# Optimization experiments

Measured on AMD Instinct MI355X. Metric: run time of the kernel, lower is better.

## Reference

```python
import jax, jax.numpy as jnp
import numpy as np

N_NODES = 20000
N_EDGES = 320000
F_DIM = 64      # num_features == hidden_units
HID = 64
N_RUNS = 10
N_GRAPHS = 128
N_CLASSES = 10
N_LAYERS = 4
BN_EPS = 1e-5
P_DROP = 0.2


def _batchnorm(t, g, b):
    # training-mode BatchNorm1d over the flattened (num_runs*N, d) rows, biased variance
    mu = jnp.mean(t, axis=0)
    var = jnp.mean(jnp.square(t - mu), axis=0)
    return (t - mu) * jax.lax.rsqrt(var + BN_EPS) * g + b


def setup_inputs() -> dict:
    key = jax.random.key(0)
    ks = jax.random.split(key, 16)
    x = jax.random.normal(ks[0], (N_NODES, F_DIM), jnp.float32)
    edge_index = jax.random.randint(ks[1], (2, N_EDGES), 0, N_NODES, dtype=jnp.int32)
    batch = jnp.sort(jax.random.randint(ks[2], (N_NODES,), 0, N_GRAPHS, dtype=jnp.int32))
    drop_mask = jax.random.uniform(ks[3], (N_RUNS, N_NODES)) < P_DROP
    s = 0.1
    conv_w1 = jax.random.normal(ks[4], (N_LAYERS, F_DIM, HID), jnp.float32) * s
    conv_b1 = jax.random.normal(ks[5], (N_LAYERS, HID), jnp.float32) * s
    bn1_g = jax.random.uniform(ks[6], (N_LAYERS, HID), jnp.float32, 0.5, 1.5)
    bn1_b = jax.random.normal(ks[7], (N_LAYERS, HID), jnp.float32) * s
    conv_w2 = jax.random.normal(ks[8], (N_LAYERS, HID, HID), jnp.float32) * s
    conv_b2 = jax.random.normal(ks[9], (N_LAYERS, HID), jnp.float32) * s
    bn_g = jax.random.uniform(ks[10], (N_LAYERS, HID), jnp.float32, 0.5, 1.5)
    bn_b = jax.random.normal(ks[11], (N_LAYERS, HID), jnp.float32) * s
    fc_w = jax.random.normal(ks[12], (N_LAYERS + 1, HID, N_CLASSES), jnp.float32) * s
    fc_b = jax.random.normal(ks[13], (N_LAYERS + 1, N_CLASSES), jnp.float32) * s
    return dict(x=x, edge_index=edge_index, batch=batch, drop_mask=drop_mask,
                conv_w1=conv_w1, conv_b1=conv_b1, bn1_g=bn1_g, bn1_b=bn1_b,
                conv_w2=conv_w2, conv_b2=conv_b2, bn_g=bn_g, bn_b=bn_b,
                fc_w=fc_w, fc_b=fc_b)


def reference(x, edge_index, batch, drop_mask,
              conv_w1, conv_b1, bn1_g, bn1_b, conv_w2, conv_b2, bn_g, bn_b,
              fc_w, fc_b):
    # prediction path (eval): node-drop, 4 GIN layers over num_runs replicated
    # graphs, per-level mean-over-runs + global_add_pool + fc, sum, log_softmax.
    R = drop_mask.shape[0]
    N = x.shape[0]
    src, dst = edge_index[0], edge_index[1]
    # replicated node features with stochastic node drop: [R, N, F]
    h = jnp.where(drop_mask[..., None], jnp.zeros((), x.dtype), x[None])
    outs = [h]
    for i in range(N_LAYERS):
        # GINConv (eps=0): MLP(x + sum_{j->i} x_j); vectorized over runs
        # (equivalent to the original offset-replicated run_edge_index).
        agg = jnp.zeros_like(h).at[:, dst].add(h[:, src])  # [R, N, d]
        z = (h + agg).reshape(R * N, -1)
        t = z @ conv_w1[i] + conv_b1[i]
        t = jax.nn.relu(_batchnorm(t, bn1_g[i], bn1_b[i]))
        t = t @ conv_w2[i] + conv_b2[i]
        t = jax.nn.relu(_batchnorm(t, bn_g[i], bn_b[i]))
        h = t.reshape(R, N, -1)
        outs.append(h)
    out = jnp.zeros((N_GRAPHS, N_CLASSES), x.dtype)
    for i, o in enumerate(outs):
        m = jnp.mean(o, axis=0)  # [N, d] mean over runs
        pooled = jax.ops.segment_sum(m, batch, num_segments=N_GRAPHS)  # global_add_pool
        out = out + pooled @ fc_w[i] + fc_b[i]  # dropout is identity in eval
    return jax.nn.log_softmax(out, axis=-1)
```

## Files before the change

kernel.cpp:

```cpp
#include <hip/hip_runtime.h>

#define N_NODES 20000
#define N_EDGES 320000
#define R_RUNS 10
#define HID 64
#define NG 128
#define NC 10
#define NL 4
#define MROWS (R_RUNS * N_NODES)
#define BN_EPS 1e-5f
#define NCOPY 16

typedef __bf16 bf16;
typedef __attribute__((ext_vector_type(8))) __bf16 bf16x8;
typedef __attribute__((ext_vector_type(4))) float f32x4;
typedef unsigned int uint32;

constexpr size_t OFF_FLAGS   = 0;
constexpr size_t OFF_CURSOR  = 256;
constexpr size_t OFF_STATS   = 80384;
constexpr size_t OFF_POOLED5 = 145920;
constexpr size_t ZERO_BYTES  = 309760;
constexpr size_t OFF_ROWST   = 309760;
constexpr size_t OFF_COL     = 389888;
constexpr size_t OFF_PARAMS  = 1669888;
constexpr size_t OFF_XB      = 1745152;
constexpr size_t OFF_H       = 4305152;
constexpr size_t OFF_Z       = 29905152;

#define PW1  0
#define PB1  16384
#define PG1  16640
#define PBB1 16896
#define PW2  17152
#define PB2  33536
#define PG2  33792
#define PBB2 34048
#define PFW  34304
#define PFB  37504
#define PTOT 37554
#define CVT_TOT (1280000 + PTOT)

__global__ void detect_kernel(const unsigned short* __restrict__ xu,
                              const unsigned int* __restrict__ mw,
                              int* __restrict__ cnts) {
    int tid = blockIdx.x * 256 + threadIdx.x;
    int insane = 0, lowp = 0, f32w = 0, gt1 = 0;
    for (int i = tid; i < 4096; i += 16384) {
        unsigned int u = xu[2 * i];
        if (((u >> 7) & 0xFFu) >= 0x90u) insane++;
    }
    for (int i = tid; i < 50000; i += 16384) {
        unsigned int w = mw[i];
        if ((w & 0xFFFFu) == 0x3F80u) lowp = 1;
        else if (w == 0x3F800000u) f32w = 1;
        else if (w > 1u) gt1 = 1;
    }
    if (insane) atomicAdd(&cnts[0], insane);
    if (lowp)   atomicOr(&cnts[1], 1);
    if (f32w)   atomicOr(&cnts[2], 1);
    if (gt1)    atomicOr(&cnts[3], 1);
}

__device__ inline bf16 ld_any(const void* p, int i, int f32mode) {
    if (f32mode) return (bf16)((const float*)p)[i];
    return ((const bf16*)p)[i];
}

__global__ void convert_kernel(const int* __restrict__ cnts,
                               const void* x, const void* w1, const void* b1,
                               const void* g1, const void* bb1, const void* w2,
                               const void* b2, const void* g2, const void* bb2,
                               const void* fw, const void* fb,
                               bf16* __restrict__ xb, bf16* __restrict__ params) {
    int t = blockIdx.x * 256 + threadIdx.x;
    if (t >= CVT_TOT) return;
    int f = cnts[0] > 64;
    if (t < 1280000) { xb[t] = ld_any(x, t, f); return; }
    int u = t - 1280000;
    if (u < PB1 || (u >= PW2 && u < PB2)) {
        const void* src = (u < PB1) ? w1 : w2;
        int v = (u < PB1) ? u : u - PW2;
        int layer = v >> 12, rem = v & 4095;
        int j = rem & 7, lane = (rem >> 3) & 63, ntc = rem >> 9;
        int nt = ntc >> 1, c = ntc & 1;
        int k = c * 32 + (lane >> 4) * 8 + j;
        int n = nt * 16 + (lane & 15);
        params[u] = ld_any(src, layer * 4096 + k * 64 + n, f);
        return;
    }
    const void* src; int base;
    if      (u < PG1)  { src = b1;  base = PB1; }
    else if (u < PBB1) { src = g1;  base = PG1; }
    else if (u < PW2)  { src = bb1; base = PBB1; }
    else if (u < PG2)  { src = b2;  base = PB2; }
    else if (u < PBB2) { src = g2;  base = PG2; }
    else if (u < PFW)  { src = bb2; base = PBB2; }
    else if (u < PFB)  { src = fw;  base = PFW; }
    else               { src = fb;  base = PFB; }
    params[u] = ld_any(src, u - base, f);
}

__global__ void build_h0_kernel(const bf16* __restrict__ xb, const void* __restrict__ maskp,
                                const int* __restrict__ cnts, bf16* __restrict__ h) {
    int i = blockIdx.x * 256 + threadIdx.x;
    int c = i & 7;
    int rowid = i >> 3;
    int r = rowid % R_RUNS;
    int n = rowid / R_RUNS;
    size_t midx = (size_t)r * N_NODES + n;
    int w = cnts[1] ? 2 : (cnts[2] ? 4 : (cnts[3] ? 1 : 4));
    int dropped;
    if (w == 1)      dropped = ((const unsigned char*)maskp)[midx] != 0;
    else if (w == 2) dropped = ((const unsigned short*)maskp)[midx] != 0;
    else             dropped = ((const unsigned int*)maskp)[midx] != 0;
    bf16x8 v;
    if (dropped) {
        #pragma unroll
        for (int j = 0; j < 8; ++j) v[j] = (bf16)0.0f;
    } else {
        v = *(const bf16x8*)(xb + (size_t)n * HID + c * 8);
    }
    *(bf16x8*)(h + (size_t)rowid * HID + c * 8) = v;
}

__global__ void csr_count_kernel(const int* __restrict__ ei, int* __restrict__ deg) {
    int e = blockIdx.x * 256 + threadIdx.x;
    if (e < N_EDGES) atomicAdd(&deg[ei[N_EDGES + e]], 1);
}

__global__ void csr_scan_kernel(int* __restrict__ deg, int* __restrict__ row_start) {
    __shared__ int lds[1024];
    int tid = threadIdx.x;
    const int CH = 20;
    int base = tid * CH;
    int local[CH];
    int s = 0;
    #pragma unroll
    for (int j = 0; j < CH; ++j) {
        int n = base + j;
        int d = (n < N_NODES) ? deg[n] : 0;
        local[j] = d; s += d;
    }
    lds[tid] = s; __syncthreads();
    for (int off = 1; off < 1024; off <<= 1) {
        int add = (tid >= off) ? lds[tid - off] : 0;
        __syncthreads();
        lds[tid] += add;
        __syncthreads();
    }
    int excl = lds[tid] - s;
    #pragma unroll
    for (int j = 0; j < CH; ++j) {
        int n = base + j;
        if (n < N_NODES) { row_start[n] = excl; deg[n] = excl; excl += local[j]; }
    }
    if (tid == 1023) row_start[N_NODES] = lds[1023];
}

__global__ void csr_fill_kernel(const int* __restrict__ ei, int* __restrict__ cursor,
                                int* __restrict__ col) {
    int e = blockIdx.x * 256 + threadIdx.x;
    if (e < N_EDGES) {
        int src = ei[e];
        int dst = ei[N_EDGES + e];
        int pos = atomicAdd(&cursor[dst], 1);
        col[pos] = src;
    }
}

__global__ __launch_bounds__(256) void agg_kernel(const uint32* __restrict__ hD,
                                                  const int* __restrict__ row_start,
                                                  const int* __restrict__ col,
                                                  uint32* __restrict__ zD) {
    int lane = threadIdx.x & 63;
    int n = blockIdx.x * 4 + (threadIdx.x >> 6);
    const int NODE_DW = R_RUNS * HID / 2;
    size_t base4 = (size_t)n * NODE_DW + lane * 4;
    size_t baset = (size_t)n * NODE_DW + 256 + lane;
    float acc[10];
    {
        uint4 u = *(const uint4*)(hD + base4);
        uint32 t = hD[baset];
        acc[0] = __uint_as_float(u.x << 16); acc[1] = __uint_as_float(u.x & 0xFFFF0000u);
        acc[2] = __uint_as_float(u.y << 16); acc[3] = __uint_as_float(u.y & 0xFFFF0000u);
        acc[4] = __uint_as_float(u.z << 16); acc[5] = __uint_as_float(u.z & 0xFFFF0000u);
        acc[6] = __uint_as_float(u.w << 16); acc[7] = __uint_as_float(u.w & 0xFFFF0000u);
        acc[8] = __uint_as_float(t << 16);   acc[9] = __uint_as_float(t & 0xFFFF0000u);
    }
    int beg = row_start[n], end = row_start[n + 1];
    int idx = beg;
    for (; idx + 4 <= end; idx += 4) {
        int s0 = col[idx], s1 = col[idx + 1], s2 = col[idx + 2], s3 = col[idx + 3];
        size_t o0 = (size_t)s0 * NODE_DW, o1 = (size_t)s1 * NODE_DW;
        size_t o2 = (size_t)s2 * NODE_DW, o3 = (size_t)s3 * NODE_DW;
        uint4 a0 = *(const uint4*)(hD + o0 + lane * 4);
        uint4 a1 = *(const uint4*)(hD + o1 + lane * 4);
        uint4 a2 = *(const uint4*)(hD + o2 + lane * 4);
        uint4 a3 = *(const uint4*)(hD + o3 + lane * 4);
        uint32 t0 = hD[o0 + 256 + lane];
        uint32 t1 = hD[o1 + 256 + lane];
        uint32 t2 = hD[o2 + 256 + lane];
        uint32 t3 = hD[o3 + 256 + lane];
        uint32 w0[4] = {a0.x, a0.y, a0.z, a0.w};
        uint32 w1[4] = {a1.x, a1.y, a1.z, a1.w};
        uint32 w2[4] = {a2.x, a2.y, a2.z, a2.w};
        uint32 w3[4] = {a3.x, a3.y, a3.z, a3.w};
        #pragma unroll
        for (int c = 0; c < 4; ++c) {
            acc[2 * c]     += __uint_as_float(w0[c] << 16) + __uint_as_float(w1[c] << 16)
                            + __uint_as_float(w2[c] << 16) + __uint_as_float(w3[c] << 16);
            acc[2 * c + 1] += __uint_as_float(w0[c] & 0xFFFF0000u) + __uint_as_float(w1[c] & 0xFFFF0000u)
                            + __uint_as_float(w2[c] & 0xFFFF0000u) + __uint_as_float(w3[c] & 0xFFFF0000u);
        }
        acc[8] += __uint_as_float(t0 << 16) + __uint_as_float(t1 << 16)
                + __uint_as_float(t2 << 16) + __uint_as_float(t3 << 16);
        acc[9] += __uint_as_float(t0 & 0xFFFF0000u) + __uint_as_float(t1 & 0xFFFF0000u)
                + __uint_as_float(t2 & 0xFFFF0000u) + __uint_as_float(t3 & 0xFFFF0000u);
    }
    for (; idx < end; ++idx) {
        size_t o0 = (size_t)col[idx] * NODE_DW;
        uint4 a0 = *(const uint4*)(hD + o0 + lane * 4);
        uint32 t0 = hD[o0 + 256 + lane];
        uint32 w0[4] = {a0.x, a0.y, a0.z, a0.w};
        #pragma unroll
        for (int c = 0; c < 4; ++c) {
            acc[2 * c]     += __uint_as_float(w0[c] << 16);
            acc[2 * c + 1] += __uint_as_float(w0[c] & 0xFFFF0000u);
        }
        acc[8] += __uint_as_float(t0 << 16);
        acc[9] += __uint_as_float(t0 & 0xFFFF0000u);
    }
    uint4 o;
    uint32 ot;
    {
        uint32 p[5];
        #pragma unroll
        for (int c = 0; c < 5; ++c) {
            unsigned short lo = __builtin_bit_cast(unsigned short, (bf16)acc[2 * c]);
            unsigned short hi = __builtin_bit_cast(unsigned short, (bf16)acc[2 * c + 1]);
            p[c] = (uint32)lo | ((uint32)hi << 16);
        }
        o.x = p[0]; o.y = p[1]; o.z = p[2]; o.w = p[3]; ot = p[4];
    }
    *(uint4*)(zD + base4) = o;
    zD[baset] = ot;
}

__global__ __launch_bounds__(256) void gemm64_kernel(const bf16* in,
                                                     const bf16* __restrict__ Wf,
                                                     const bf16* __restrict__ bias,
                                                     bf16* out,
                                                     const float* __restrict__ statsIn,
                                                     const bf16* __restrict__ gammaIn,
                                                     const bf16* __restrict__ betaIn,
                                                     float* __restrict__ statsOut) {
    __shared__ float lstat[128];
    __shared__ float lscale[64], lshift[64];
    __shared__ float lsum[64], lsq[64];
    int tid = threadIdx.x;
    int wave = tid >> 6, lane = tid & 63, l16 = lane & 15, quad = lane >> 4;

    if (statsIn) {
        if (tid < 128) {
            float s = 0.f;
            #pragma unroll
            for (int k = 0; k < NCOPY; ++k) s += statsIn[k * 128 + tid];
            lstat[tid] = s;
        }
    }
    if (tid < 64) { lsum[tid] = 0.f; lsq[tid] = 0.f; }
    __syncthreads();
    if (statsIn && tid < 64) {
        float mu = lstat[tid] * (1.0f / MROWS);
        float var = lstat[tid + 64] * (1.0f / MROWS) - mu * mu;
        float rs = rsqrtf(var + BN_EPS);
        float a = (float)gammaIn[tid] * rs;
        lscale[tid] = a;
        lshift[tid] = (float)betaIn[tid] - mu * a;
    }
    if (statsIn) __syncthreads();

    size_t rowBase = (size_t)blockIdx.x * 64 + wave * 16;

    bf16x8 bfrag[4][2];
    #pragma unroll
    for (int nt = 0; nt < 4; ++nt)
        #pragma unroll
        for (int c = 0; c < 2; ++c)
            bfrag[nt][c] = *(const bf16x8*)(Wf + (size_t)((nt * 2 + c) * 64 + lane) * 8);

    f32x4 acc[4];
    #pragma unroll
    for (int nt = 0; nt < 4; ++nt) {
        float bv = (float)bias[nt * 16 + l16];
        acc[nt] = (f32x4){bv, bv, bv, bv};
    }

    size_t row = rowBase + l16;
    bf16x8 afrag[2];
    #pragma unroll
    for (int c = 0; c < 2; ++c) {
        int k0 = c * 32 + quad * 8;
        bf16x8 v = *(const bf16x8*)(in + row * HID + k0);
        if (statsIn) {
            #pragma unroll
            for (int j = 0; j < 8; ++j) {
                float f = (float)v[j] * lscale[k0 + j] + lshift[k0 + j];
                v[j] = (bf16)fmaxf(f, 0.f);
            }
        }
        afrag[c] = v;
    }

    #pragma unroll
    for (int nt = 0; nt < 4; ++nt) {
        acc[nt] = __builtin_amdgcn_mfma_f32_16x16x32_bf16(afrag[0], bfrag[nt][0], acc[nt], 0, 0, 0);
        acc[nt] = __builtin_amdgcn_mfma_f32_16x16x32_bf16(afrag[1], bfrag[nt][1], acc[nt], 0, 0, 0);
    }

    #pragma unroll
    for (int nt = 0; nt < 4; ++nt)
        #pragma unroll
        for (int reg = 0; reg < 4; ++reg) {
            size_t orow = rowBase + quad * 4 + reg;
            out[orow * HID + nt * 16 + l16] = (bf16)acc[nt][reg];
        }

    #pragma unroll
    for (int nt = 0; nt < 4; ++nt) {
        float s = 0.f, q = 0.f;
        #pragma unroll
        for (int reg = 0; reg < 4; ++reg) { float v = acc[nt][reg]; s += v; q += v * v; }
        atomicAdd(&lsum[nt * 16 + l16], s);
        atomicAdd(&lsq[nt * 16 + l16], q);
    }
    __syncthreads();
    if (tid < 64) {
        int copy = blockIdx.x & (NCOPY - 1);
        atomicAdd(&statsOut[copy * 128 + tid], lsum[tid]);
        atomicAdd(&statsOut[copy * 128 + 64 + tid], lsq[tid]);
    }
}

__global__ __launch_bounds__(256) void pool_bn_kernel(const bf16* __restrict__ t,
                                                      const float* __restrict__ statsIn,
                                                      const bf16* __restrict__ gammaIn,
                                                      const bf16* __restrict__ betaIn,
                                                      bf16* __restrict__ hOut,
                                                      const int* __restrict__ batch,
                                                      float* __restrict__ pooled) {
    __shared__ float lstat[128], lscale[64], lshift[64];
    int tid = threadIdx.x;
    if (statsIn) {
        if (tid < 128) {
            float s = 0.f;
            #pragma unroll
            for (int k = 0; k < NCOPY; ++k) s += statsIn[k * 128 + tid];
            lstat[tid] = s;
        }
        __syncthreads();
        if (tid < 64) {
            float mu = lstat[tid] * (1.0f / MROWS);
            float var = lstat[tid + 64] * (1.0f / MROWS) - mu * mu;
            float rs = rsqrtf(var + BN_EPS);
            float a = (float)gammaIn[tid] * rs;
            lscale[tid] = a;
            lshift[tid] = (float)betaIn[tid] - mu * a;
        }
        __syncthreads();
    }
    int gid = blockIdx.x * 256 + tid;
    int f = tid & 63, n = gid >> 6;
    float sc = statsIn ? lscale[f] : 1.f;
    float sh = statsIn ? lshift[f] : 0.f;
    size_t base = (size_t)n * (R_RUNS * HID) + f;
    float s = 0.f;
    #pragma unroll
    for (int r = 0; r < R_RUNS; ++r) {
        float v = (float)t[base + r * HID];
        if (statsIn) {
            v = fmaxf(v * sc + sh, 0.f);
            hOut[base + r * HID] = (bf16)v;
        }
        s += v;
    }
    atomicAdd(&pooled[batch[n] * HID + f], s * (1.0f / R_RUNS));
}

__global__ void fc_softmax_kernel(const float* __restrict__ pooled5,
                                  const bf16* __restrict__ params,
                                  const int* __restrict__ cnts, void* __restrict__ out) {
    int g = threadIdx.x;
    if (g >= NG) return;
    float o[NC];
    #pragma unroll
    for (int c = 0; c < NC; ++c) o[c] = 0.f;
    for (int l = 0; l < NL + 1; ++l) {
        const float* pg = pooled5 + ((size_t)l * NG + g) * HID;
        const bf16* fw = params + PFW + l * (HID * NC);
        for (int k = 0; k < HID; ++k) {
            float p = pg[k];
            #pragma unroll
            for (int c = 0; c < NC; ++c) o[c] += p * (float)fw[k * NC + c];
        }
        #pragma unroll
        for (int c = 0; c < NC; ++c) o[c] += (float)params[PFB + l * NC + c];
    }
    float m = -1e30f;
    #pragma unroll
    for (int c = 0; c < NC; ++c) m = fmaxf(m, o[c]);
    float s = 0.f;
    #pragma unroll
    for (int c = 0; c < NC; ++c) s += expf(o[c] - m);
    float lg = logf(s);
    int f = cnts[0] > 64;
    #pragma unroll
    for (int c = 0; c < NC; ++c) {
        float val = o[c] - m - lg;
        if (f) ((float*)out)[g * NC + c] = val;
        else   ((bf16*)out)[g * NC + c] = (bf16)val;
    }
}

extern "C" void kernel_launch(void* const* d_in, const int* in_sizes, int n_in,
                              void* d_out, int out_size, void* d_ws, size_t ws_size,
                              hipStream_t stream) {
    const void* x     = d_in[0];
    const int*  ei    = (const int*)d_in[1];
    const int*  batch = (const int*)d_in[2];
    const void* maskp = d_in[3];

    char* ws = (char*)d_ws;
    int*   cnts    = (int*)(ws + OFF_FLAGS);
    int*   cursor  = (int*)(ws + OFF_CURSOR);
    float* statsb  = (float*)(ws + OFF_STATS);
    float* pooled5 = (float*)(ws + OFF_POOLED5);
    int*   rowst   = (int*)(ws + OFF_ROWST);
    int*   colbuf  = (int*)(ws + OFF_COL);
    bf16*  params  = (bf16*)(ws + OFF_PARAMS);
    bf16*  xb      = (bf16*)(ws + OFF_XB);
    bf16*  h       = (bf16*)(ws + OFF_H);
    bf16*  z       = (bf16*)(ws + OFF_Z);

    hipMemsetAsync(ws, 0, ZERO_BYTES, stream);

    detect_kernel<<<64, 256, 0, stream>>>((const unsigned short*)x,
                                          (const unsigned int*)maskp, cnts);
    convert_kernel<<<(CVT_TOT + 255) / 256, 256, 0, stream>>>(
        cnts, x, d_in[4], d_in[5], d_in[6], d_in[7], d_in[8], d_in[9], d_in[10],
        d_in[11], d_in[12], d_in[13], xb, params);

    build_h0_kernel<<<(MROWS * 8) / 256, 256, 0, stream>>>(xb, maskp, cnts, h);

    csr_count_kernel<<<(N_EDGES + 255) / 256, 256, 0, stream>>>(ei, cursor);
    csr_scan_kernel<<<1, 1024, 0, stream>>>(cursor, rowst);
    csr_fill_kernel<<<(N_EDGES + 255) / 256, 256, 0, stream>>>(ei, cursor, colbuf);

    pool_bn_kernel<<<(N_NODES * HID) / 256, 256, 0, stream>>>(
        h, nullptr, nullptr, nullptr, nullptr, batch, pooled5);

    for (int i = 0; i < NL; ++i) {
        float* st1 = statsb + (size_t)(2 * i) * (NCOPY * 128);
        float* st2 = statsb + (size_t)(2 * i + 1) * (NCOPY * 128);

        agg_kernel<<<N_NODES / 4, 256, 0, stream>>>((const uint32*)h, rowst, colbuf,
                                                    (uint32*)z);

        gemm64_kernel<<<MROWS / 64, 256, 0, stream>>>(
            z, params + PW1 + i * 4096, params + PB1 + i * 64, z,
            nullptr, nullptr, nullptr, st1);

        gemm64_kernel<<<MROWS / 64, 256, 0, stream>>>(
            z, params + PW2 + i * 4096, params + PB2 + i * 64, z,
            st1, params + PG1 + i * 64, params + PBB1 + i * 64, st2);

        pool_bn_kernel<<<(N_NODES * HID) / 256, 256, 0, stream>>>(
            z, st2, params + PG2 + i * 64, params + PBB2 + i * 64, h, batch,
            pooled5 + (size_t)(i + 1) * NG * HID);
    }

    fc_softmax_kernel<<<1, 128, 0, stream>>>(pooled5, params, cnts, d_out);
}
```

Measured before the change: 869.0 us.

## Fuse per-layer GEMMs, BatchNorm and pooling into one persistent kernel with grid barriers

Replaces the two gemm64 launches and the pool_bn launch per layer with a single persistent layer_kernel of 500 blocks. Each block keeps its 400-row intermediate tile in shared memory and uses software grid barriers to wait for the global BatchNorm statistics. This removes two round trips of the intermediate activations through global memory and two launches per layer. The agg kernel's gather loop is also unrolled to 8 independent loads per iteration for more memory-level parallelism. The grid barrier assumes all 500 blocks are co-resident, and the large shared tile per block may limit occupancy.

```diff
diff --git a/kernel.cpp b/kernel.cpp
--- a/kernel.cpp
+++ b/kernel.cpp
@@ -10,6 +10,9 @@
 #define MROWS (R_RUNS * N_NODES)
 #define BN_EPS 1e-5f
 #define NCOPY 16
+#define NPB 40
+#define GRID_L 500
+#define TSTRIDE 66
 
 typedef __bf16 bf16;
 typedef __attribute__((ext_vector_type(8))) __bf16 bf16x8;
@@ -17,16 +20,17 @@
 typedef unsigned int uint32;
 
 constexpr size_t OFF_FLAGS   = 0;
-constexpr size_t OFF_CURSOR  = 256;
-constexpr size_t OFF_STATS   = 80384;
-constexpr size_t OFF_POOLED5 = 145920;
-constexpr size_t ZERO_BYTES  = 309760;
-constexpr size_t OFF_ROWST   = 309760;
-constexpr size_t OFF_COL     = 389888;
-constexpr size_t OFF_PARAMS  = 1669888;
-constexpr size_t OFF_XB      = 1745152;
-constexpr size_t OFF_H       = 4305152;
-constexpr size_t OFF_Z       = 29905152;
+constexpr size_t OFF_BARRIER = 256;
+constexpr size_t OFF_CURSOR  = 768;
+constexpr size_t OFF_STATS   = 81152;
+constexpr size_t OFF_POOLED5 = 146688;
+constexpr size_t ZERO_BYTES  = 310528;
+constexpr size_t OFF_ROWST   = 310528;
+constexpr size_t OFF_COL     = 390912;
+constexpr size_t OFF_PARAMS  = 1670912;
+constexpr size_t OFF_XB      = 1746176;
+constexpr size_t OFF_H       = 4306176;
+constexpr size_t OFF_Z       = 29906176;
 
 #define PW1  0
 #define PB1  16384
@@ -190,33 +194,45 @@
     }
     int beg = row_start[n], end = row_start[n + 1];
     int idx = beg;
+    for (; idx + 8 <= end; idx += 8) {
+        uint4 a[8]; uint32 t[8];
+        #pragma unroll
+        for (int u = 0; u < 8; ++u) {
+            size_t o = (size_t)col[idx + u] * NODE_DW;
+            a[u] = *(const uint4*)(hD + o + lane * 4);
+            t[u] = hD[o + 256 + lane];
+        }
+        #pragma unroll
+        for (int u = 0; u < 8; ++u) {
+            uint32 w[4] = {a[u].x, a[u].y, a[u].z, a[u].w};
+            #pragma unroll
+            for (int c = 0; c < 4; ++c) {
+                acc[2 * c]     += __uint_as_float(w[c] << 16);
+                acc[2 * c + 1] += __uint_as_float(w[c] & 0xFFFF0000u);
+            }
+            acc[8] += __uint_as_float(t[u] << 16);
+            acc[9] += __uint_as_float(t[u] & 0xFFFF0000u);
+        }
+    }
     for (; idx + 4 <= end; idx += 4) {
-        int s0 = col[idx], s1 = col[idx + 1], s2 = col[idx + 2], s3 = col[idx + 3];
-        size_t o0 = (size_t)s0 * NODE_DW, o1 = (size_t)s1 * NODE_DW;
-        size_t o2 = (size_t)s2 * NODE_DW, o3 = (size_t)s3 * NODE_DW;
-        uint4 a0 = *(const uint4*)(hD + o0 + lane * 4);
-        uint4 a1 = *(const uint4*)(hD + o1 + lane * 4);
-        uint4 a2 = *(const uint4*)(hD + o2 + lane * 4);
-        uint4 a3 = *(const uint4*)(hD + o3 + lane * 4);
-        uint32 t0 = hD[o0 + 256 + lane];
-        uint32 t1 = hD[o1 + 256 + lane];
-        uint32 t2 = hD[o2 + 256 + lane];
-        uint32 t3 = hD[o3 + 256 + lane];
-        uint32 w0[4] = {a0.x, a0.y, a0.z, a0.w};
-        uint32 w1[4] = {a1.x, a1.y, a1.z, a1.w};
-        uint32 w2[4] = {a2.x, a2.y, a2.z, a2.w};
-        uint32 w3[4] = {a3.x, a3.y, a3.z, a3.w};
-        #pragma unroll
-        for (int c = 0; c < 4; ++c) {
-            acc[2 * c]     += __uint_as_float(w0[c] << 16) + __uint_as_float(w1[c] << 16)
-                            + __uint_as_float(w2[c] << 16) + __uint_as_float(w3[c] << 16);
-            acc[2 * c + 1] += __uint_as_float(w0[c] & 0xFFFF0000u) + __uint_as_float(w1[c] & 0xFFFF0000u)
-                            + __uint_as_float(w2[c] & 0xFFFF0000u) + __uint_as_float(w3[c] & 0xFFFF0000u);
-        }
-        acc[8] += __uint_as_float(t0 << 16) + __uint_as_float(t1 << 16)
-                + __uint_as_float(t2 << 16) + __uint_as_float(t3 << 16);
-        acc[9] += __uint_as_float(t0 & 0xFFFF0000u) + __uint_as_float(t1 & 0xFFFF0000u)
-                + __uint_as_float(t2 & 0xFFFF0000u) + __uint_as_float(t3 & 0xFFFF0000u);
+        uint4 a[4]; uint32 t[4];
+        #pragma unroll
+        for (int u = 0; u < 4; ++u) {
+            size_t o = (size_t)col[idx + u] * NODE_DW;
+            a[u] = *(const uint4*)(hD + o + lane * 4);
+            t[u] = hD[o + 256 + lane];
+        }
+        #pragma unroll
+        for (int u = 0; u < 4; ++u) {
+            uint32 w[4] = {a[u].x, a[u].y, a[u].z, a[u].w};
+            #pragma unroll
+            for (int c = 0; c < 4; ++c) {
+                acc[2 * c]     += __uint_as_float(w[c] << 16);
+                acc[2 * c + 1] += __uint_as_float(w[c] & 0xFFFF0000u);
+            }
+            acc[8] += __uint_as_float(t[u] << 16);
+            acc[9] += __uint_as_float(t[u] & 0xFFFF0000u);
+        }
     }
     for (; idx < end; ++idx) {
         size_t o0 = (size_t)col[idx] * NODE_DW;
@@ -231,8 +247,7 @@
         acc[8] += __uint_as_float(t0 << 16);
         acc[9] += __uint_as_float(t0 & 0xFFFF0000u);
     }
-    uint4 o;
-    uint32 ot;
+    uint4 o; uint32 ot;
     {
         uint32 p[5];
         #pragma unroll
@@ -247,144 +262,211 @@
     zD[baset] = ot;
 }
 
-__global__ __launch_bounds__(256) void gemm64_kernel(const bf16* in,
-                                                     const bf16* __restrict__ Wf,
-                                                     const bf16* __restrict__ bias,
-                                                     bf16* out,
-                                                     const float* __restrict__ statsIn,
-                                                     const bf16* __restrict__ gammaIn,
-                                                     const bf16* __restrict__ betaIn,
-                                                     float* __restrict__ statsOut) {
-    __shared__ float lstat[128];
-    __shared__ float lscale[64], lshift[64];
-    __shared__ float lsum[64], lsq[64];
+__device__ inline void grid_barrier(int* ctr, int nblocks) {
+    __syncthreads();
+    if (threadIdx.x == 0) {
+        __threadfence();
+        __hip_atomic_fetch_add(ctr, 1, __ATOMIC_ACQ_REL, __HIP_MEMORY_SCOPE_AGENT);
+        while (__hip_atomic_load(ctr, __ATOMIC_ACQUIRE, __HIP_MEMORY_SCOPE_AGENT) < nblocks)
+            __builtin_amdgcn_s_sleep(16);
+    }
+    __syncthreads();
+}
+
+__global__ __launch_bounds__(256) void layer_kernel(const bf16* __restrict__ z,
+                                                    const bf16* __restrict__ params,
+                                                    int layer,
+                                                    bf16* __restrict__ hNext,
+                                                    const int* __restrict__ batch,
+                                                    float* __restrict__ st1,
+                                                    float* __restrict__ st2,
+                                                    float* __restrict__ pooled,
+                                                    int* __restrict__ bar) {
+    __shared__ bf16 tT[NPB * R_RUNS * TSTRIDE];
+    __shared__ float lstat[128], lscale[64], lshift[64], lsum[64], lsq[64];
     int tid = threadIdx.x;
     int wave = tid >> 6, lane = tid & 63, l16 = lane & 15, quad = lane >> 4;
-
-    if (statsIn) {
-        if (tid < 128) {
-            float s = 0.f;
+    int b = blockIdx.x;
+
+    const bf16* Wf1 = params + PW1 + layer * 4096;
+    const bf16* Wf2 = params + PW2 + layer * 4096;
+    const bf16* bi1 = params + PB1 + layer * 64;
+    const bf16* bi2 = params + PB2 + layer * 64;
+    const bf16* ga1 = params + PG1 + layer * 64;
+    const bf16* be1 = params + PBB1 + layer * 64;
+    const bf16* ga2 = params + PG2 + layer * 64;
+    const bf16* be2 = params + PBB2 + layer * 64;
+
+    if (tid < 64) { lsum[tid] = 0.f; lsq[tid] = 0.f; }
+    __syncthreads();
+
+    {
+        bf16x8 bfr[4][2];
+        #pragma unroll
+        for (int nt = 0; nt < 4; ++nt)
             #pragma unroll
-            for (int k = 0; k < NCOPY; ++k) s += statsIn[k * 128 + tid];
-            lstat[tid] = s;
-        }
-    }
+            for (int c = 0; c < 2; ++c)
+                bfr[nt][c] = *(const bf16x8*)(Wf1 + (size_t)((nt * 2 + c) * 64 + lane) * 8);
+        for (int g = wave; g < 5; g += 4) {
+            int rL0 = g * 80;
+            size_t rG0 = (size_t)b * (NPB * R_RUNS) + rL0;
+            for (int s = 0; s < 5; ++s) {
+                size_t row = rG0 + s * 16 + l16;
+                bf16x8 a0 = *(const bf16x8*)(z + row * HID + quad * 8);
+                bf16x8 a1 = *(const bf16x8*)(z + row * HID + 32 + quad * 8);
+                f32x4 acc[4];
+                #pragma unroll
+                for (int nt = 0; nt < 4; ++nt) {
+                    float bv = (float)bi1[nt * 16 + l16];
+                    acc[nt] = (f32x4){bv, bv, bv, bv};
+                }
+                #pragma unroll
+                for (int nt = 0; nt < 4; ++nt) {
+                    acc[nt] = __builtin_amdgcn_mfma_f32_16x16x32_bf16(a0, bfr[nt][0], acc[nt], 0, 0, 0);
+                    acc[nt] = __builtin_amdgcn_mfma_f32_16x16x32_bf16(a1, bfr[nt][1], acc[nt], 0, 0, 0);
+                }
+                int rL = rL0 + s * 16;
+                #pragma unroll
+                for (int nt = 0; nt < 4; ++nt) {
+                    float ss = 0.f, qq = 0.f;
+                    #pragma unroll
+                    for (int reg = 0; reg < 4; ++reg) {
+                        float v = acc[nt][reg];
+                        ss += v; qq += v * v;
+                        tT[(rL + quad * 4 + reg) * TSTRIDE + nt * 16 + l16] = (bf16)v;
+                    }
+                    atomicAdd(&lsum[nt * 16 + l16], ss);
+                    atomicAdd(&lsq[nt * 16 + l16], qq);
+                }
+            }
+        }
+    }
+    __syncthreads();
+    if (tid < 64) {
+        int copy = b & (NCOPY - 1);
+        atomicAdd(&st1[copy * 128 + tid], lsum[tid]);
+        atomicAdd(&st1[copy * 128 + 64 + tid], lsq[tid]);
+    }
+    __syncthreads();
     if (tid < 64) { lsum[tid] = 0.f; lsq[tid] = 0.f; }
-    __syncthreads();
-    if (statsIn && tid < 64) {
+    grid_barrier(&bar[0], GRID_L);
+
+    if (tid < 128) {
+        float s = 0.f;
+        #pragma unroll
+        for (int k = 0; k < NCOPY; ++k)
+            s += __hip_atomic_load(&st1[k * 128 + tid], __ATOMIC_RELAXED, __HIP_MEMORY_SCOPE_AGENT);
+        lstat[tid] = s;
+    }
+    __syncthreads();
+    if (tid < 64) {
         float mu = lstat[tid] * (1.0f / MROWS);
         float var = lstat[tid + 64] * (1.0f / MROWS) - mu * mu;
         float rs = rsqrtf(var + BN_EPS);
-        float a = (float)gammaIn[tid] * rs;
+        float a = (float)ga1[tid] * rs;
         lscale[tid] = a;
-        lshift[tid] = (float)betaIn[tid] - mu * a;
-    }
-    if (statsIn) __syncthreads();
-
-    size_t rowBase = (size_t)blockIdx.x * 64 + wave * 16;
-
-    bf16x8 bfrag[4][2];
-    #pragma unroll
-    for (int nt = 0; nt < 4; ++nt)
-        #pragma unroll
-        for (int c = 0; c < 2; ++c)
-            bfrag[nt][c] = *(const bf16x8*)(Wf + (size_t)((nt * 2 + c) * 64 + lane) * 8);
-
-    f32x4 acc[4];
-    #pragma unroll
-    for (int nt = 0; nt < 4; ++nt) {
-        float bv = (float)bias[nt * 16 + l16];
-        acc[nt] = (f32x4){bv, bv, bv, bv};
-    }
-
-    size_t row = rowBase + l16;
-    bf16x8 afrag[2];
-    #pragma unroll
-    for (int c = 0; c < 2; ++c) {
-        int k0 = c * 32 + quad * 8;
-        bf16x8 v = *(const bf16x8*)(in + row * HID + k0);
-        if (statsIn) {
+        lshift[tid] = (float)be1[tid] - mu * a;
+    }
+    __syncthreads();
+
+    {
+        bf16x8 bfr[4][2];
+        #pragma unroll
+        for (int nt = 0; nt < 4; ++nt)
             #pragma unroll
-            for (int j = 0; j < 8; ++j) {
-                float f = (float)v[j] * lscale[k0 + j] + lshift[k0 + j];
-                v[j] = (bf16)fmaxf(f, 0.f);
+            for (int c = 0; c < 2; ++c)
+                bfr[nt][c] = *(const bf16x8*)(Wf2 + (size_t)((nt * 2 + c) * 64 + lane) * 8);
+        for (int g = wave; g < 5; g += 4) {
+            int rL0 = g * 80;
+            for (int s = 0; s < 5; ++s) {
+                int rL = rL0 + s * 16;
+                const bf16* tp = &tT[(rL + l16) * TSTRIDE];
+                bf16x8 a0 = *(const bf16x8*)(tp + quad * 8);
+                bf16x8 a1 = *(const bf16x8*)(tp + 32 + quad * 8);
+                #pragma unroll
+                for (int j = 0; j < 8; ++j) {
+                    int k0 = quad * 8 + j, k1 = 32 + quad * 8 + j;
+                    a0[j] = (bf16)fmaxf((float)a0[j] * lscale[k0] + lshift[k0], 0.f);
+                    a1[j] = (bf16)fmaxf((float)a1[j] * lscale[k1] + lshift[k1], 0.f);
+                }
+                f32x4 acc[4];
+                #pragma unroll
+                for (int nt = 0; nt < 4; ++nt) {
+                    float bv = (float)bi2[nt * 16 + l16];
+                    acc[nt] = (f32x4){bv, bv, bv, bv};
+                }
+                #pragma unroll
+                for (int nt = 0; nt < 4; ++nt) {
+                    acc[nt] = __builtin_amdgcn_mfma_f32_16x16x32_bf16(a0, bfr[nt][0], acc[nt], 0, 0, 0);
+                    acc[nt] = __builtin_amdgcn_mfma_f32_16x16x32_bf16(a1, bfr[nt][1], acc[nt], 0, 0, 0);
+                }
+                #pragma unroll
+                for (int nt = 0; nt < 4; ++nt) {
+                    float ss = 0.f, qq = 0.f;
+                    #pragma unroll
+                    for (int reg = 0; reg < 4; ++reg) {
+                        float v = acc[nt][reg];
+                        ss += v; qq += v * v;
+                        tT[(rL + quad * 4 + reg) * TSTRIDE + nt * 16 + l16] = (bf16)v;
+                    }
+                    atomicAdd(&lsum[nt * 16 + l16], ss);
+                    atomicAdd(&lsq[nt * 16 + l16], qq);
+                }
             }
         }
-        afrag[c] = v;
-    }
-
-    #pragma unroll
-    for (int nt = 0; nt < 4; ++nt) {
-        acc[nt] = __builtin_amdgcn_mfma_f32_16x16x32_bf16(afrag[0], bfrag[nt][0], acc[nt], 0, 0, 0);
-        acc[nt] = __builtin_amdgcn_mfma_f32_16x16x32_bf16(afrag[1], bfrag[nt][1], acc[nt], 0, 0, 0);
-    }
-
-    #pragma unroll
-    for (int nt = 0; nt < 4; ++nt)
-        #pragma unroll
-        for (int reg = 0; reg < 4; ++reg) {
-            size_t orow = rowBase + quad * 4 + reg;
-            out[orow * HID + nt * 16 + l16] = (bf16)acc[nt][reg];
-        }
-
-    #pragma unroll
-    for (int nt = 0; nt < 4; ++nt) {
-        float s = 0.f, q = 0.f;
-        #pragma unroll
-        for (int reg = 0; reg < 4; ++reg) { float v = acc[nt][reg]; s += v; q += v * v; }
-        atomicAdd(&lsum[nt * 16 + l16], s);
-        atomicAdd(&lsq[nt * 16 + l16], q);
     }
     __syncthreads();
     if (tid < 64) {
-        int copy = blockIdx.x & (NCOPY - 1);
-        atomicAdd(&statsOut[copy * 128 + tid], lsum[tid]);
-        atomicAdd(&statsOut[copy * 128 + 64 + tid], lsq[tid]);
-    }
-}
-
-__global__ __launch_bounds__(256) void pool_bn_kernel(const bf16* __restrict__ t,
-                                                      const float* __restrict__ statsIn,
-                                                      const bf16* __restrict__ gammaIn,
-                                                      const bf16* __restrict__ betaIn,
-                                                      bf16* __restrict__ hOut,
-                                                      const int* __restrict__ batch,
-                                                      float* __restrict__ pooled) {
-    __shared__ float lstat[128], lscale[64], lshift[64];
-    int tid = threadIdx.x;
-    if (statsIn) {
-        if (tid < 128) {
-            float s = 0.f;
-            #pragma unroll
-            for (int k = 0; k < NCOPY; ++k) s += statsIn[k * 128 + tid];
-            lstat[tid] = s;
-        }
-        __syncthreads();
-        if (tid < 64) {
-            float mu = lstat[tid] * (1.0f / MROWS);
-            float var = lstat[tid + 64] * (1.0f / MROWS) - mu * mu;
-            float rs = rsqrtf(var + BN_EPS);
-            float a = (float)gammaIn[tid] * rs;
-            lscale[tid] = a;
-            lshift[tid] = (float)betaIn[tid] - mu * a;
-        }
-        __syncthreads();
-    }
-    int gid = blockIdx.x * 256 + tid;
-    int f = tid & 63, n = gid >> 6;
-    float sc = statsIn ? lscale[f] : 1.f;
-    float sh = statsIn ? lshift[f] : 0.f;
+        int copy = b & (NCOPY - 1);
+        atomicAdd(&st2[copy * 128 + tid], lsum[tid]);
+        atomicAdd(&st2[copy * 128 + 64 + tid], lsq[tid]);
+    }
+    grid_barrier(&bar[1], GRID_L);
+
+    if (tid < 128) {
+        float s = 0.f;
+        #pragma unroll
+        for (int k = 0; k < NCOPY; ++k)
+            s += __hip_atomic_load(&st2[k * 128 + tid], __ATOMIC_RELAXED, __HIP_MEMORY_SCOPE_AGENT);
+        lstat[tid] = s;
+    }
+    __syncthreads();
+    if (tid < 64) {
+        float mu = lstat[tid] * (1.0f / MROWS);
+        float var = lstat[tid + 64] * (1.0f / MROWS) - mu * mu;
+        float rs = rsqrtf(var + BN_EPS);
+        float a = (float)ga2[tid] * rs;
+        lscale[tid] = a;
+        lshift[tid] = (float)be2[tid] - mu * a;
+    }
+    __syncthreads();
+
+    for (int it = 0; it < (NPB * HID) / 256; ++it) {
+        int idx = it * 256 + tid;
+        int nl = idx >> 6, f = idx & 63;
+        float sc = lscale[f], sh = lshift[f];
+        size_t gRow = ((size_t)b * NPB + nl) * R_RUNS;
+        float s = 0.f;
+        #pragma unroll
+        for (int r = 0; r < R_RUNS; ++r) {
+            float v = (float)tT[(nl * R_RUNS + r) * TSTRIDE + f];
+            v = fmaxf(v * sc + sh, 0.f);
+            hNext[(gRow + r) * HID + f] = (bf16)v;
+            s += v;
+        }
+        atomicAdd(&pooled[batch[b * NPB + nl] * HID + f], s * (1.0f / R_RUNS));
+    }
+}
+
+__global__ __launch_bounds__(256) void pool0_kernel(const bf16* __restrict__ t,
+                                                    const int* __restrict__ batch,
+                                                    float* __restrict__ pooled) {
+    int gid = blockIdx.x * 256 + threadIdx.x;
+    int f = gid & 63, n = gid >> 6;
     size_t base = (size_t)n * (R_RUNS * HID) + f;
     float s = 0.f;
     #pragma unroll
-    for (int r = 0; r < R_RUNS; ++r) {
-        float v = (float)t[base + r * HID];
-        if (statsIn) {
-            v = fmaxf(v * sc + sh, 0.f);
-            hOut[base + r * HID] = (bf16)v;
-        }
-        s += v;
-    }
+    for (int r = 0; r < R_RUNS; ++r) s += (float)t[base + r * HID];
     atomicAdd(&pooled[batch[n] * HID + f], s * (1.0f / R_RUNS));
 }
 
@@ -433,6 +515,7 @@
 
     char* ws = (char*)d_ws;
     int*   cnts    = (int*)(ws + OFF_FLAGS);
+    int*   barc    = (int*)(ws + OFF_BARRIER);
     int*   cursor  = (int*)(ws + OFF_CURSOR);
     float* statsb  = (float*)(ws + OFF_STATS);
     float* pooled5 = (float*)(ws + OFF_POOLED5);
@@ -457,8 +540,7 @@
     csr_scan_kernel<<<1, 1024, 0, stream>>>(cursor, rowst);
     csr_fill_kernel<<<(N_EDGES + 255) / 256, 256, 0, stream>>>(ei, cursor, colbuf);
 
-    pool_bn_kernel<<<(N_NODES * HID) / 256, 256, 0, stream>>>(
-        h, nullptr, nullptr, nullptr, nullptr, batch, pooled5);
+    pool0_kernel<<<(N_NODES * HID) / 256, 256, 0, stream>>>(h, batch, pooled5);
 
     for (int i = 0; i < NL; ++i) {
         float* st1 = statsb + (size_t)(2 * i) * (NCOPY * 128);
@@ -467,17 +549,9 @@
         agg_kernel<<<N_NODES / 4, 256, 0, stream>>>((const uint32*)h, rowst, colbuf,
                                                     (uint32*)z);
 
-        gemm64_kernel<<<MROWS / 64, 256, 0, stream>>>(
-            z, params + PW1 + i * 4096, params + PB1 + i * 64, z,
-            nullptr, nullptr, nullptr, st1);
-
-        gemm64_kernel<<<MROWS / 64, 256, 0, stream>>>(
-            z, params + PW2 + i * 4096, params + PB2 + i * 64, z,
-            st1, params + PG1 + i * 64, params + PBB1 + i * 64, st2);
-
-        pool_bn_kernel<<<(N_NODES * HID) / 256, 256, 0, stream>>>(
-            z, st2, params + PG2 + i * 64, params + PBB2 + i * 64, h, batch,
-            pooled5 + (size_t)(i + 1) * NG * HID);
+        layer_kernel<<<GRID_L, 256, 0, stream>>>(
+            z, params, i, h, batch, st1, st2,
+            pooled5 + (size_t)(i + 1) * NG * HID, barc + 2 * i);
     }
 
     fc_softmax_kernel<<<1, 128, 0, stream>>>(pooled5, params, cnts, d_out);
```

After: 1.049 ms. 1.21x slower.

## Fuse neighbor aggregation with first GEMM and merge h0 build with pooling

Applied to the files above, without the earlier changes.

The CSR aggregation is fused with the first MLP linear layer. Each block aggregates 16 nodes (160 rows across runs) into an LDS tile, then runs MFMA against W1 and accumulates BatchNorm statistics, so the z round trip through global memory between the aggregation and GEMM1 kernels goes away. Building the initial dropped-node features is also merged with the level-0 mean-over-runs pooling, which removes one pass over h. The price is extra LDS use and fewer, heavier blocks for the gather stage, which could lower occupancy or latency hiding.

```diff
diff --git a/kernel.cpp b/kernel.cpp
--- a/kernel.cpp
+++ b/kernel.cpp
@@ -10,6 +10,7 @@
 #define MROWS (R_RUNS * N_NODES)
 #define BN_EPS 1e-5f
 #define NCOPY 16
+#define TS 72
 
 typedef __bf16 bf16;
 typedef __attribute__((ext_vector_type(8))) __bf16 bf16x8;
@@ -18,15 +19,15 @@
 
 constexpr size_t OFF_FLAGS   = 0;
 constexpr size_t OFF_CURSOR  = 256;
-constexpr size_t OFF_STATS   = 80384;
-constexpr size_t OFF_POOLED5 = 145920;
-constexpr size_t ZERO_BYTES  = 309760;
-constexpr size_t OFF_ROWST   = 309760;
-constexpr size_t OFF_COL     = 389888;
-constexpr size_t OFF_PARAMS  = 1669888;
-constexpr size_t OFF_XB      = 1745152;
-constexpr size_t OFF_H       = 4305152;
-constexpr size_t OFF_Z       = 29905152;
+constexpr size_t OFF_STATS   = 80640;
+constexpr size_t OFF_POOLED5 = 146176;
+constexpr size_t ZERO_BYTES  = 310016;
+constexpr size_t OFF_ROWST   = 310016;
+constexpr size_t OFF_COL     = 390400;
+constexpr size_t OFF_PARAMS  = 1670400;
+constexpr size_t OFF_XB      = 1745664;
+constexpr size_t OFF_H       = 4305664;
+constexpr size_t OFF_Z       = 29905664;
 
 #define PW1  0
 #define PB1  16384
@@ -101,27 +102,38 @@
     params[u] = ld_any(src, u - base, f);
 }
 
-__global__ void build_h0_kernel(const bf16* __restrict__ xb, const void* __restrict__ maskp,
-                                const int* __restrict__ cnts, bf16* __restrict__ h) {
-    int i = blockIdx.x * 256 + threadIdx.x;
-    int c = i & 7;
-    int rowid = i >> 3;
-    int r = rowid % R_RUNS;
-    int n = rowid / R_RUNS;
-    size_t midx = (size_t)r * N_NODES + n;
+__global__ void build_h0_pool_kernel(const bf16* __restrict__ xb,
+                                     const void* __restrict__ maskp,
+                                     const int* __restrict__ cnts,
+                                     const int* __restrict__ batch,
+                                     bf16* __restrict__ h,
+                                     float* __restrict__ pooled) {
+    int t = blockIdx.x * 256 + threadIdx.x;
+    int c = t & 7, n = t >> 3;
     int w = cnts[1] ? 2 : (cnts[2] ? 4 : (cnts[3] ? 1 : 4));
-    int dropped;
-    if (w == 1)      dropped = ((const unsigned char*)maskp)[midx] != 0;
-    else if (w == 2) dropped = ((const unsigned short*)maskp)[midx] != 0;
-    else             dropped = ((const unsigned int*)maskp)[midx] != 0;
-    bf16x8 v;
-    if (dropped) {
-        #pragma unroll
-        for (int j = 0; j < 8; ++j) v[j] = (bf16)0.0f;
-    } else {
-        v = *(const bf16x8*)(xb + (size_t)n * HID + c * 8);
-    }
-    *(bf16x8*)(h + (size_t)rowid * HID + c * 8) = v;
+    bf16x8 xv = *(const bf16x8*)(xb + (size_t)n * HID + c * 8);
+    bf16x8 zv;
+    #pragma unroll
+    for (int j = 0; j < 8; ++j) zv[j] = (bf16)0.0f;
+    float s[8];
+    #pragma unroll
+    for (int j = 0; j < 8; ++j) s[j] = 0.f;
+    #pragma unroll
+    for (int r = 0; r < R_RUNS; ++r) {
+        size_t midx = (size_t)r * N_NODES + n;
+        int dropped;
+        if (w == 1)      dropped = ((const unsigned char*)maskp)[midx] != 0;
+        else if (w == 2) dropped = ((const unsigned short*)maskp)[midx] != 0;
+        else             dropped = ((const unsigned int*)maskp)[midx] != 0;
+        *(bf16x8*)(h + ((size_t)n * R_RUNS + r) * HID + c * 8) = dropped ? zv : xv;
+        if (!dropped)
+            #pragma unroll
+            for (int j = 0; j < 8; ++j) s[j] += (float)xv[j];
+    }
+    int g = batch[n];
+    #pragma unroll
+    for (int j = 0; j < 8; ++j)
+        atomicAdd(&pooled[g * HID + c * 8 + j], s[j] * (1.0f / R_RUNS));
 }
 
 __global__ void csr_count_kernel(const int* __restrict__ ei, int* __restrict__ deg) {
@@ -169,82 +181,127 @@
     }
 }
 
-__global__ __launch_bounds__(256) void agg_kernel(const uint32* __restrict__ hD,
+__global__ __launch_bounds__(256) void ag1_kernel(const uint32* __restrict__ hD,
                                                   const int* __restrict__ row_start,
                                                   const int* __restrict__ col,
-                                                  uint32* __restrict__ zD) {
-    int lane = threadIdx.x & 63;
-    int n = blockIdx.x * 4 + (threadIdx.x >> 6);
+                                                  const bf16* __restrict__ Wf,
+                                                  const bf16* __restrict__ bias,
+                                                  bf16* __restrict__ out,
+                                                  float* __restrict__ statsOut) {
+    __shared__ __align__(16) bf16 zT[16 * R_RUNS * TS];
+    __shared__ float lsum[64], lsq[64];
+    uint32* zTu = (uint32*)zT;
+    int tid = threadIdx.x;
+    int wave = tid >> 6, lane = tid & 63, l16 = lane & 15, quad = lane >> 4;
+    int b = blockIdx.x;
     const int NODE_DW = R_RUNS * HID / 2;
-    size_t base4 = (size_t)n * NODE_DW + lane * 4;
-    size_t baset = (size_t)n * NODE_DW + 256 + lane;
-    float acc[10];
-    {
-        uint4 u = *(const uint4*)(hD + base4);
-        uint32 t = hD[baset];
-        acc[0] = __uint_as_float(u.x << 16); acc[1] = __uint_as_float(u.x & 0xFFFF0000u);
-        acc[2] = __uint_as_float(u.y << 16); acc[3] = __uint_as_float(u.y & 0xFFFF0000u);
-        acc[4] = __uint_as_float(u.z << 16); acc[5] = __uint_as_float(u.z & 0xFFFF0000u);
-        acc[6] = __uint_as_float(u.w << 16); acc[7] = __uint_as_float(u.w & 0xFFFF0000u);
-        acc[8] = __uint_as_float(t << 16);   acc[9] = __uint_as_float(t & 0xFFFF0000u);
-    }
-    int beg = row_start[n], end = row_start[n + 1];
-    int idx = beg;
-    for (; idx + 4 <= end; idx += 4) {
-        int s0 = col[idx], s1 = col[idx + 1], s2 = col[idx + 2], s3 = col[idx + 3];
-        size_t o0 = (size_t)s0 * NODE_DW, o1 = (size_t)s1 * NODE_DW;
-        size_t o2 = (size_t)s2 * NODE_DW, o3 = (size_t)s3 * NODE_DW;
-        uint4 a0 = *(const uint4*)(hD + o0 + lane * 4);
-        uint4 a1 = *(const uint4*)(hD + o1 + lane * 4);
-        uint4 a2 = *(const uint4*)(hD + o2 + lane * 4);
-        uint4 a3 = *(const uint4*)(hD + o3 + lane * 4);
-        uint32 t0 = hD[o0 + 256 + lane];
-        uint32 t1 = hD[o1 + 256 + lane];
-        uint32 t2 = hD[o2 + 256 + lane];
-        uint32 t3 = hD[o3 + 256 + lane];
-        uint32 w0[4] = {a0.x, a0.y, a0.z, a0.w};
-        uint32 w1[4] = {a1.x, a1.y, a1.z, a1.w};
-        uint32 w2[4] = {a2.x, a2.y, a2.z, a2.w};
-        uint32 w3[4] = {a3.x, a3.y, a3.z, a3.w};
-        #pragma unroll
-        for (int c = 0; c < 4; ++c) {
-            acc[2 * c]     += __uint_as_float(w0[c] << 16) + __uint_as_float(w1[c] << 16)
-                            + __uint_as_float(w2[c] << 16) + __uint_as_float(w3[c] << 16);
-            acc[2 * c + 1] += __uint_as_float(w0[c] & 0xFFFF0000u) + __uint_as_float(w1[c] & 0xFFFF0000u)
-                            + __uint_as_float(w2[c] & 0xFFFF0000u) + __uint_as_float(w3[c] & 0xFFFF0000u);
-        }
-        acc[8] += __uint_as_float(t0 << 16) + __uint_as_float(t1 << 16)
-                + __uint_as_float(t2 << 16) + __uint_as_float(t3 << 16);
-        acc[9] += __uint_as_float(t0 & 0xFFFF0000u) + __uint_as_float(t1 & 0xFFFF0000u)
-                + __uint_as_float(t2 & 0xFFFF0000u) + __uint_as_float(t3 & 0xFFFF0000u);
-    }
-    for (; idx < end; ++idx) {
-        size_t o0 = (size_t)col[idx] * NODE_DW;
-        uint4 a0 = *(const uint4*)(hD + o0 + lane * 4);
-        uint32 t0 = hD[o0 + 256 + lane];
-        uint32 w0[4] = {a0.x, a0.y, a0.z, a0.w};
-        #pragma unroll
-        for (int c = 0; c < 4; ++c) {
-            acc[2 * c]     += __uint_as_float(w0[c] << 16);
-            acc[2 * c + 1] += __uint_as_float(w0[c] & 0xFFFF0000u);
-        }
-        acc[8] += __uint_as_float(t0 << 16);
-        acc[9] += __uint_as_float(t0 & 0xFFFF0000u);
-    }
-    uint4 o;
-    uint32 ot;
-    {
-        uint32 p[5];
+
+    if (tid < 64) { lsum[tid] = 0.f; lsq[tid] = 0.f; }
+
+    for (int i = 0; i < 4; ++i) {
+        int nl = wave + 4 * i;
+        int n = b * 16 + nl;
+        size_t base4 = (size_t)n * NODE_DW + lane * 4;
+        size_t baset = (size_t)n * NODE_DW + 256 + lane;
+        float acc[10];
+        {
+            uint4 u = *(const uint4*)(hD + base4);
+            uint32 tw = hD[baset];
+            acc[0] = __uint_as_float(u.x << 16); acc[1] = __uint_as_float(u.x & 0xFFFF0000u);
+            acc[2] = __uint_as_float(u.y << 16); acc[3] = __uint_as_float(u.y & 0xFFFF0000u);
+            acc[4] = __uint_as_float(u.z << 16); acc[5] = __uint_as_float(u.z & 0xFFFF0000u);
+            acc[6] = __uint_as_float(u.w << 16); acc[7] = __uint_as_float(u.w & 0xFFFF0000u);
+            acc[8] = __uint_as_float(tw << 16);  acc[9] = __uint_as_float(tw & 0xFFFF0000u);
+        }
+        int beg = row_start[n], end = row_start[n + 1];
+        int idx = beg;
+        for (; idx + 4 <= end; idx += 4) {
+            uint4 a[4]; uint32 tw[4];
+            #pragma unroll
+            for (int u = 0; u < 4; ++u) {
+                size_t o = (size_t)col[idx + u] * NODE_DW;
+                a[u] = *(const uint4*)(hD + o + lane * 4);
+                tw[u] = hD[o + 256 + lane];
+            }
+            #pragma unroll
+            for (int u = 0; u < 4; ++u) {
+                uint32 wd[4] = {a[u].x, a[u].y, a[u].z, a[u].w};
+                #pragma unroll
+                for (int c = 0; c < 4; ++c) {
+                    acc[2 * c]     += __uint_as_float(wd[c] << 16);
+                    acc[2 * c + 1] += __uint_as_float(wd[c] & 0xFFFF0000u);
+                }
+                acc[8] += __uint_as_float(tw[u] << 16);
+                acc[9] += __uint_as_float(tw[u] & 0xFFFF0000u);
+            }
+        }
+        for (; idx < end; ++idx) {
+            size_t o = (size_t)col[idx] * NODE_DW;
+            uint4 a0 = *(const uint4*)(hD + o + lane * 4);
+            uint32 t0 = hD[o + 256 + lane];
+            uint32 wd[4] = {a0.x, a0.y, a0.z, a0.w};
+            #pragma unroll
+            for (int c = 0; c < 4; ++c) {
+                acc[2 * c]     += __uint_as_float(wd[c] << 16);
+                acc[2 * c + 1] += __uint_as_float(wd[c] & 0xFFFF0000u);
+            }
+            acc[8] += __uint_as_float(t0 << 16);
+            acc[9] += __uint_as_float(t0 & 0xFFFF0000u);
+        }
         #pragma unroll
         for (int c = 0; c < 5; ++c) {
+            int d = (c < 4) ? (lane * 4 + c) : (256 + lane);
+            int rL = nl * R_RUNS + (d >> 5);
+            int fp = d & 31;
             unsigned short lo = __builtin_bit_cast(unsigned short, (bf16)acc[2 * c]);
             unsigned short hi = __builtin_bit_cast(unsigned short, (bf16)acc[2 * c + 1]);
-            p[c] = (uint32)lo | ((uint32)hi << 16);
-        }
-        o.x = p[0]; o.y = p[1]; o.z = p[2]; o.w = p[3]; ot = p[4];
-    }
-    *(uint4*)(zD + base4) = o;
-    zD[baset] = ot;
+            zTu[rL * (TS / 2) + fp] = (uint32)lo | ((uint32)hi << 16);
+        }
+    }
+    __syncthreads();
+
+    bf16x8 bfr[4][2];
+    #pragma unroll
+    for (int nt = 0; nt < 4; ++nt)
+        #pragma unroll
+        for (int c = 0; c < 2; ++c)
+            bfr[nt][c] = *(const bf16x8*)(Wf + (size_t)((nt * 2 + c) * 64 + lane) * 8);
+    float bvs[4];
+    #pragma unroll
+    for (int nt = 0; nt < 4; ++nt) bvs[nt] = (float)bias[nt * 16 + l16];
+
+    for (int g = wave; g < 10; g += 4) {
+        const bf16* tp = &zT[(g * 16 + l16) * TS];
+        bf16x8 a0 = *(const bf16x8*)(tp + quad * 8);
+        bf16x8 a1 = *(const bf16x8*)(tp + 32 + quad * 8);
+        f32x4 acc[4];
+        #pragma unroll
+        for (int nt = 0; nt < 4; ++nt) acc[nt] = (f32x4){bvs[nt], bvs[nt], bvs[nt], bvs[nt]};
+        #pragma unroll
+        for (int nt = 0; nt < 4; ++nt) {
+            acc[nt] = __builtin_amdgcn_mfma_f32_16x16x32_bf16(a0, bfr[nt][0], acc[nt], 0, 0, 0);
+            acc[nt] = __builtin_amdgcn_mfma_f32_16x16x32_bf16(a1, bfr[nt][1], acc[nt], 0, 0, 0);
+        }
+        size_t rowBase = (size_t)b * 160 + g * 16;
+        #pragma unroll
+        for (int nt = 0; nt < 4; ++nt) {
+            float ss = 0.f, qq = 0.f;
+            #pragma unroll
+            for (int reg = 0; reg < 4; ++reg) {
+                float v = acc[nt][reg];
+                ss += v; qq += v * v;
+                out[(rowBase + quad * 4 + reg) * HID + nt * 16 + l16] = (bf16)v;
+            }
+            atomicAdd(&lsum[nt * 16 + l16], ss);
+            atomicAdd(&lsq[nt * 16 + l16], qq);
+        }
+    }
+    __syncthreads();
+    if (tid < 64) {
+        int copy = b & (NCOPY - 1);
+        atomicAdd(&statsOut[copy * 128 + tid], lsum[tid]);
+        atomicAdd(&statsOut[copy * 128 + 64 + tid], lsq[tid]);
+    }
 }
 
 __global__ __launch_bounds__(256) void gemm64_kernel(const bf16* in,
@@ -261,17 +318,15 @@
     int tid = threadIdx.x;
     int wave = tid >> 6, lane = tid & 63, l16 = lane & 15, quad = lane >> 4;
 
-    if (statsIn) {
-        if (tid < 128) {
-            float s = 0.f;
-            #pragma unroll
-            for (int k = 0; k < NCOPY; ++k) s += statsIn[k * 128 + tid];
-            lstat[tid] = s;
-        }
+    if (tid < 128) {
+        float s = 0.f;
+        #pragma unroll
+        for (int k = 0; k < NCOPY; ++k) s += statsIn[k * 128 + tid];
+        lstat[tid] = s;
     }
     if (tid < 64) { lsum[tid] = 0.f; lsq[tid] = 0.f; }
     __syncthreads();
-    if (statsIn && tid < 64) {
+    if (tid < 64) {
         float mu = lstat[tid] * (1.0f / MROWS);
         float var = lstat[tid + 64] * (1.0f / MROWS) - mu * mu;
         float rs = rsqrtf(var + BN_EPS);
@@ -279,7 +334,7 @@
         lscale[tid] = a;
         lshift[tid] = (float)betaIn[tid] - mu * a;
     }
-    if (statsIn) __syncthreads();
+    __syncthreads();
 
     size_t rowBase = (size_t)blockIdx.x * 64 + wave * 16;
 
@@ -303,12 +358,10 @@
     for (int c = 0; c < 2; ++c) {
         int k0 = c * 32 + quad * 8;
         bf16x8 v = *(const bf16x8*)(in + row * HID + k0);
-        if (statsIn) {
-            #pragma unroll
-            for (int j = 0; j < 8; ++j) {
-                float f = (float)v[j] * lscale[k0 + j] + lshift[k0 + j];
-                v[j] = (bf16)fmaxf(f, 0.f);
-            }
+        #pragma unroll
+        for (int j = 0; j < 8; ++j) {
+            float f = (float)v[j] * lscale[k0 + j] + lshift[k0 + j];
+            v[j] = (bf16)fmaxf(f, 0.f);
         }
         afrag[c] = v;
     }
@@ -352,37 +405,32 @@
                                                       float* __restrict__ pooled) {
     __shared__ float lstat[128], lscale[64], lshift[64];
     int tid = threadIdx.x;
-    if (statsIn) {
-        if (tid < 128) {
-            float s = 0.f;
-            #pragma unroll
-            for (int k = 0; k < NCOPY; ++k) s += statsIn[k * 128 + tid];
-            lstat[tid] = s;
-        }
-        __syncthreads();
-        if (tid < 64) {
-            float mu = lstat[tid] * (1.0f / MROWS);
-            float var = lstat[tid + 64] * (1.0f / MROWS) - mu * mu;
-            float rs = rsqrtf(var + BN_EPS);
-            float a = (float)gammaIn[tid] * rs;
-            lscale[tid] = a;
-            lshift[tid] = (float)betaIn[tid] - mu * a;
-        }
-        __syncthreads();
-    }
+    if (tid < 128) {
+        float s = 0.f;
+        #pragma unroll
+        for (int k = 0; k < NCOPY; ++k) s += statsIn[k * 128 + tid];
+        lstat[tid] = s;
+    }
+    __syncthreads();
+    if (tid < 64) {
+        float mu = lstat[tid] * (1.0f / MROWS);
+        float var = lstat[tid + 64] * (1.0f / MROWS) - mu * mu;
+        float rs = rsqrtf(var + BN_EPS);
+        float a = (float)gammaIn[tid] * rs;
+        lscale[tid] = a;
+        lshift[tid] = (float)betaIn[tid] - mu * a;
+    }
+    __syncthreads();
     int gid = blockIdx.x * 256 + tid;
     int f = tid & 63, n = gid >> 6;
-    float sc = statsIn ? lscale[f] : 1.f;
-    float sh = statsIn ? lshift[f] : 0.f;
+    float sc = lscale[f], sh = lshift[f];
     size_t base = (size_t)n * (R_RUNS * HID) + f;
     float s = 0.f;
     #pragma unroll
     for (int r = 0; r < R_RUNS; ++r) {
         float v = (float)t[base + r * HID];
-        if (statsIn) {
-            v = fmaxf(v * sc + sh, 0.f);
-            hOut[base + r * HID] = (bf16)v;
-        }
+        v = fmaxf(v * sc + sh, 0.f);
+        hOut[base + r * HID] = (bf16)v;
         s += v;
     }
     atomicAdd(&pooled[batch[n] * HID + f], s * (1.0f / R_RUNS));
@@ -451,25 +499,20 @@
         cnts, x, d_in[4], d_in[5], d_in[6], d_in[7], d_in[8], d_in[9], d_in[10],
         d_in[11], d_in[12], d_in[13], xb, params);
 
-    build_h0_kernel<<<(MROWS * 8) / 256, 256, 0, stream>>>(xb, maskp, cnts, h);
-
     csr_count_kernel<<<(N_EDGES + 255) / 256, 256, 0, stream>>>(ei, cursor);
     csr_scan_kernel<<<1, 1024, 0, stream>>>(cursor, rowst);
     csr_fill_kernel<<<(N_EDGES + 255) / 256, 256, 0, stream>>>(ei, cursor, colbuf);
 
-    pool_bn_kernel<<<(N_NODES * HID) / 256, 256, 0, stream>>>(
-        h, nullptr, nullptr, nullptr, nullptr, batch, pooled5);
+    build_h0_pool_kernel<<<(N_NODES * 8) / 256, 256, 0, stream>>>(
+        xb, maskp, cnts, batch, h, pooled5);
 
     for (int i = 0; i < NL; ++i) {
         float* st1 = statsb + (size_t)(2 * i) * (NCOPY * 128);
         float* st2 = statsb + (size_t)(2 * i + 1) * (NCOPY * 128);
 
-        agg_kernel<<<N_NODES / 4, 256, 0, stream>>>((const uint32*)h, rowst, colbuf,
-                                                    (uint32*)z);
-
-        gemm64_kernel<<<MROWS / 64, 256, 0, stream>>>(
-            z, params + PW1 + i * 4096, params + PB1 + i * 64, z,
-            nullptr, nullptr, nullptr, st1);
+        ag1_kernel<<<N_NODES / 16, 256, 0, stream>>>(
+            (const uint32*)h, rowst, colbuf,
+            params + PW1 + i * 4096, params + PB1 + i * 64, z, st1);
 
         gemm64_kernel<<<MROWS / 64, 256, 0, stream>>>(
             z, params + PW2 + i * 4096, params + PB2 + i * 64, z,
```

Result: slower. 887.0 us (+2.1%).
